# Optimization experiments

Hardware: AMD Instinct MI355X
Metric: run time of the kernel (lower is better)

The kernel has to match this reference:

```python
import jax, jax.numpy as jnp
import numpy as np

INPUT_DIM = 2048
N_EXPERTS = 64
K = 2


def setup_inputs() -> dict:
    key = jax.random.key(0)
    kx, kw, kb = jax.random.split(key, 3)
    x = jax.random.normal(kx, (4, 4096, INPUT_DIM), dtype=jnp.float32)
    # nn.Linear(input_dim, n_experts): weight [n_experts, input_dim], bias [n_experts]
    bound = 1.0 / np.sqrt(INPUT_DIM)
    W = jax.random.uniform(kw, (N_EXPERTS, INPUT_DIM), minval=-bound, maxval=bound, dtype=jnp.float32)
    b = jax.random.uniform(kb, (N_EXPERTS,), minval=-bound, maxval=bound, dtype=jnp.float32)
    return {"x": x, "W": W, "b": b}


def reference(x, W, b):
    # logits: [B, S, E]
    logits = jnp.einsum('bsd,ed->bse', x, W) + b
    topk_vals, topk_indices = jax.lax.top_k(logits, K)  # over last (expert) axis
    gate_probs = jax.nn.softmax(topk_vals, axis=-1)
    return gate_probs, topk_indices
```

## Files before the change

kernel.cpp:

```cpp
#include <hip/hip_runtime.h>
#include <math.h>
#include <stdint.h>

typedef _Float16 half8 __attribute__((ext_vector_type(8)));
typedef float floatx4 __attribute__((ext_vector_type(4)));

#define NTOK   16384
#define DIM    2048
#define NEXP   64
#define MB     32
#define NBLK   (NTOK / MB)
#define KC     64
#define NCHUNK (DIM / KC)
#define WSW_H8 16384
#define WSW_BYTES (2 * WSW_H8 * 16)

#define A_BYTES 8192
#define B_BYTES 16384
#define AOFF(b) ((b) * A_BYTES)
#define BOFF(b) (2 * A_BYTES + (b) * B_BYTES)
#define SMEM_BYTES (2 * A_BYTES + 2 * B_BYTES)

__global__ void wprep_kernel(const float* __restrict__ W, _Float16* __restrict__ wsw) {
    const int id   = blockIdx.x * blockDim.x + threadIdx.x;
    const int lane = id & 63;
    const int tg   = (id >> 6) & 3;
    const int sg   = id >> 8;
    const int e    = tg * 16 + (lane & 15);
    const int k    = sg * 32 + (lane >> 4) * 8;
    const float* src = W + (size_t)e * DIM + k;
    half8 h, l;
#pragma unroll
    for (int j = 0; j < 8; j++) {
        const float v  = src[j];
        const _Float16 hh = (_Float16)v;
        h[j] = hh;
        l[j] = (_Float16)((v - (float)hh) * 2048.0f);
    }
    const size_t slot = (size_t)(sg * 4 + tg) * 64 + lane;
    ((half8*)wsw)[slot]          = h;
    ((half8*)wsw)[WSW_H8 + slot] = l;
}

__device__ __forceinline__ void split_a(const float4& v0, const float4& v1,
                                        half8& hi, half8& lo) {
    const float av[8] = {v0.x, v0.y, v0.z, v0.w, v1.x, v1.y, v1.z, v1.w};
#pragma unroll
    for (int j = 0; j < 8; j++) {
        const _Float16 hh = (_Float16)av[j];
        hi[j] = hh;
        lo[j] = (_Float16)((av[j] - (float)hh) * 2048.0f);
    }
}

__device__ __forceinline__ void dma16(const void* g, const char* l) {
    __builtin_amdgcn_global_load_lds(
        (const __attribute__((address_space(1))) unsigned int*)(uintptr_t)g,
        (__attribute__((address_space(3))) unsigned int*)(uintptr_t)l,
        16, 0, 0);
}

template <bool USE_WS>
__global__ __launch_bounds__(256, 3)
void gating_lds_kernel(const float* __restrict__ x, const float* __restrict__ W,
                       const _Float16* __restrict__ wsw, const float* __restrict__ bias,
                       float* __restrict__ out)
{
    __shared__ char smem[SMEM_BYTES];

    const int tid  = threadIdx.x;
    const int lane = tid & 63;
    const int w    = tid >> 6;
    const int mt   = w & 1;
    const int nh   = w >> 1;
    const int col  = lane & 15;
    const int quad = lane >> 4;
    const int tok0 = blockIdx.x * MB;
    const int m    = mt * 16 + col;

    const float* gA[2];
    unsigned     lA[2];
#pragma unroll
    for (int i = 0; i < 2; i++) {
        const int a   = w * 2 + i;
        const int row = a * 4 + (lane >> 4);
        const int pz  = lane & 15;
        const int gp  = (pz & 8) | ((pz & 7) ^ (row & 7));
        gA[i] = x + (size_t)(tok0 + row) * DIM + gp * 4;
        lA[i] = (unsigned)(a * 1024);
    }
    const half8* gB[4];
    unsigned     lB[4];
    if constexpr (USE_WS) {
#pragma unroll
        for (int j = 0; j < 4; j++) {
            const int b = w * 4 + j;
            const int split = b >> 3, idx = b & 7;
            gB[j] = (const half8*)wsw + (size_t)split * WSW_H8 + idx * 64 + lane;
            lB[j] = (unsigned)(split * 8192 + idx * 1024);
        }
    }

    floatx4 accm[2] = {{0,0,0,0},{0,0,0,0}};
    floatx4 accl[2] = {{0,0,0,0},{0,0,0,0}};

#pragma unroll
    for (int i = 0; i < 2; i++) dma16(gA[i], smem + AOFF(0) + lA[i]);
    if constexpr (USE_WS) {
#pragma unroll
        for (int j = 0; j < 4; j++) dma16(gB[j], smem + BOFF(0) + lB[j]);
    }

#pragma unroll 2
    for (int c = 0; c < NCHUNK; ++c) {
        __syncthreads();
        if (c + 1 < NCHUNK) {
            const int nb = (c + 1) & 1;
#pragma unroll
            for (int i = 0; i < 2; i++)
                dma16(gA[i] + (size_t)(c + 1) * KC, smem + AOFF(nb) + lA[i]);
            if constexpr (USE_WS) {
#pragma unroll
                for (int j = 0; j < 4; j++)
                    dma16(gB[j] + (size_t)(c + 1) * 512, smem + BOFF(nb) + lB[j]);
            }
        }
        const char* Ab = smem + AOFF(c & 1);
        const char* Bb = smem + BOFF(c & 1);
#pragma unroll
        for (int s = 0; s < 2; s++) {
            const float4 v0 = *(const float4*)(Ab + m * 256 + (8 * s + ((2 * quad + 0) ^ (m & 7))) * 16);
            const float4 v1 = *(const float4*)(Ab + m * 256 + (8 * s + ((2 * quad + 1) ^ (m & 7))) * 16);
            half8 ah, alo;
            split_a(v0, v1, ah, alo);
#pragma unroll
            for (int t = 0; t < 2; t++) {
                const int tg = nh * 2 + t;
                half8 bh, bl;
                if constexpr (USE_WS) {
                    bh = *(const half8*)(Bb + (s * 4 + tg) * 1024 + lane * 16);
                    bl = *(const half8*)(Bb + 8192 + (s * 4 + tg) * 1024 + lane * 16);
                } else {
                    const float* wr = W + (size_t)(tg * 16 + col) * DIM + c * KC + s * 32 + quad * 8;
                    split_a(*(const float4*)wr, *(const float4*)(wr + 4), bh, bl);
                }
                accm[t] = __builtin_amdgcn_mfma_f32_16x16x32_f16(ah,  bh, accm[t], 0, 0, 0);
                accl[t] = __builtin_amdgcn_mfma_f32_16x16x32_f16(ah,  bl, accl[t], 0, 0, 0);
                accl[t] = __builtin_amdgcn_mfma_f32_16x16x32_f16(alo, bh, accl[t], 0, 0, 0);
            }
        }
    }

    __syncthreads();
    float* lg = (float*)smem;
    const float inv = 1.0f / 2048.0f;
#pragma unroll
    for (int t = 0; t < 2; t++) {
        const int tg = nh * 2 + t;
#pragma unroll
        for (int r = 0; r < 4; r++) {
            lg[(mt * 16 + quad * 4 + r) * 65 + tg * 16 + col] = accm[t][r] + accl[t][r] * inv;
        }
    }
    __syncthreads();

    if (tid < MB) {
        const int t = tid;
        float v0 = -INFINITY, v1 = -INFINITY;
        int   i0 = 0, i1 = 0;
        for (int e = 0; e < NEXP; e++) {
            const float v = lg[t * 65 + e] + bias[e];
            if (v > v0) { v1 = v0; i1 = i0; v0 = v; i0 = e; }
            else if (v > v1) { v1 = v; i1 = e; }
        }
        const float e1 = expf(v1 - v0);
        const float sden = 1.f + e1;
        const int   g  = tok0 + t;
        out[2 * g + 0] = 1.f / sden;
        out[2 * g + 1] = e1 / sden;
        out[2 * NTOK + 2 * g + 0] = (float)i0;
        out[2 * NTOK + 2 * g + 1] = (float)i1;
    }
}

extern "C" void kernel_launch(void* const* d_in, const int* in_sizes, int n_in,
                              void* d_out, int out_size, void* d_ws, size_t ws_size,
                              hipStream_t stream) {
    const float* x    = (const float*)d_in[0];
    const float* W    = (const float*)d_in[1];
    const float* bias = (const float*)d_in[2];
    float*       out  = (float*)d_out;
    _Float16*    wsw  = (_Float16*)d_ws;

    if (ws_size >= (size_t)WSW_BYTES) {
        hipLaunchKernelGGL(wprep_kernel, dim3(64), dim3(256), 0, stream, (const float*)d_in[1], wsw);
        hipLaunchKernelGGL((gating_lds_kernel<true>), dim3(NBLK), dim3(256), 0, stream,
                           x, W, wsw, bias, out);
    } else {
        hipLaunchKernelGGL((gating_lds_kernel<false>), dim3(NBLK), dim3(256), 0, stream,
                           x, W, wsw, bias, out);
    }
}
```

Measured before the change: 207.1 us.

## Split K across waves with register-held W fragments and LDS reduction

Each block now handles 16 tokens, and each of its four waves owns a quarter of the K dimension across all 64 experts, instead of splitting tokens and experts among waves. The pre-split W fragments are loaded straight into registers with a one-chunk prefetch rather than staged through LDS. Per-wave x tiles are double-buffered with DMA and synchronized only by explicit vmcnt waits, so there are no block barriers inside the loop. Partial logits are reduced through LDS before the top-2 step. The aim is to remove per-chunk __syncthreads and LDS traffic for W, at the cost of more registers, twice as many blocks, redundant W reads per block, and fragile hand-counted vmcnt values.

```diff
diff --git a/kernel.cpp b/kernel.cpp
--- a/kernel.cpp
+++ b/kernel.cpp
@@ -8,18 +8,15 @@
 #define NTOK   16384
 #define DIM    2048
 #define NEXP   64
-#define MB     32
-#define NBLK   (NTOK / MB)
-#define KC     64
-#define NCHUNK (DIM / KC)
+#define TPB    16
+#define NBLK   (NTOK / TPB)
+#define NCHW   8
 #define WSW_H8 16384
 #define WSW_BYTES (2 * WSW_H8 * 16)
 
-#define A_BYTES 8192
-#define B_BYTES 16384
-#define AOFF(b) ((b) * A_BYTES)
-#define BOFF(b) (2 * A_BYTES + (b) * B_BYTES)
-#define SMEM_BYTES (2 * A_BYTES + 2 * B_BYTES)
+#define ABUF_BYTES 32768
+#define RED_STRIDE 68
+#define RED_F      (4 * 16 * RED_STRIDE)
 
 __global__ void wprep_kernel(const float* __restrict__ W, _Float16* __restrict__ wsw) {
     const int id   = blockIdx.x * blockDim.x + threadIdx.x;
@@ -60,122 +57,137 @@
         16, 0, 0);
 }
 
+template <bool USE_WS> struct BFrag;
+template <> struct BFrag<true>  { half8  h[2][4]; half8 l[2][4]; };
+template <> struct BFrag<false> { float4 a[2][4][2]; };
+
+template <bool USE_WS>
+__device__ __forceinline__ void load_b(BFrag<USE_WS>& bf, const half8* wb,
+                                       const float* Wb, int cc) {
+    if constexpr (USE_WS) {
+#pragma unroll
+        for (int s = 0; s < 2; s++)
+#pragma unroll
+            for (int t = 0; t < 4; t++) {
+                const size_t o = (size_t)(cc * 8 + s * 4 + t) * 64;
+                bf.h[s][t] = wb[o];
+                bf.l[s][t] = wb[o + WSW_H8];
+            }
+    } else {
+#pragma unroll
+        for (int s = 0; s < 2; s++)
+#pragma unroll
+            for (int t = 0; t < 4; t++) {
+                const float* wr = Wb + (size_t)(t * 16) * DIM + cc * 64 + s * 32;
+                bf.a[s][t][0] = *(const float4*)wr;
+                bf.a[s][t][1] = *(const float4*)(wr + 4);
+            }
+    }
+}
+
 template <bool USE_WS>
 __global__ __launch_bounds__(256, 3)
-void gating_lds_kernel(const float* __restrict__ x, const float* __restrict__ W,
-                       const _Float16* __restrict__ wsw, const float* __restrict__ bias,
-                       float* __restrict__ out)
+void gating_kernel(const float* __restrict__ x, const float* __restrict__ W,
+                   const _Float16* __restrict__ wsw, const float* __restrict__ bias,
+                   float* __restrict__ out)
 {
-    __shared__ char smem[SMEM_BYTES];
+    __shared__ char  abuf[ABUF_BYTES];
+    __shared__ float red[RED_F];
 
     const int tid  = threadIdx.x;
     const int lane = tid & 63;
-    const int w    = tid >> 6;
-    const int mt   = w & 1;
-    const int nh   = w >> 1;
+    const int ks   = tid >> 6;
     const int col  = lane & 15;
     const int quad = lane >> 4;
-    const int tok0 = blockIdx.x * MB;
-    const int m    = mt * 16 + col;
-
-    const float* gA[2];
-    unsigned     lA[2];
-#pragma unroll
-    for (int i = 0; i < 2; i++) {
-        const int a   = w * 2 + i;
-        const int row = a * 4 + (lane >> 4);
-        const int pz  = lane & 15;
+    const int tok0 = blockIdx.x * TPB;
+
+    const float* gA[4];
+#pragma unroll
+    for (int i = 0; i < 4; i++) {
+        const int row = i * 4 + quad;
+        const int pz  = col;
         const int gp  = (pz & 8) | ((pz & 7) ^ (row & 7));
-        gA[i] = x + (size_t)(tok0 + row) * DIM + gp * 4;
-        lA[i] = (unsigned)(a * 1024);
-    }
-    const half8* gB[4];
-    unsigned     lB[4];
-    if constexpr (USE_WS) {
-#pragma unroll
-        for (int j = 0; j < 4; j++) {
-            const int b = w * 4 + j;
-            const int split = b >> 3, idx = b & 7;
-            gB[j] = (const half8*)wsw + (size_t)split * WSW_H8 + idx * 64 + lane;
-            lB[j] = (unsigned)(split * 8192 + idx * 1024);
-        }
-    }
-
-    floatx4 accm[2] = {{0,0,0,0},{0,0,0,0}};
-    floatx4 accl[2] = {{0,0,0,0},{0,0,0,0}};
-
-#pragma unroll
-    for (int i = 0; i < 2; i++) dma16(gA[i], smem + AOFF(0) + lA[i]);
-    if constexpr (USE_WS) {
-#pragma unroll
-        for (int j = 0; j < 4; j++) dma16(gB[j], smem + BOFF(0) + lB[j]);
-    }
-
-#pragma unroll 2
-    for (int c = 0; c < NCHUNK; ++c) {
-        __syncthreads();
-        if (c + 1 < NCHUNK) {
-            const int nb = (c + 1) & 1;
-#pragma unroll
-            for (int i = 0; i < 2; i++)
-                dma16(gA[i] + (size_t)(c + 1) * KC, smem + AOFF(nb) + lA[i]);
-            if constexpr (USE_WS) {
-#pragma unroll
-                for (int j = 0; j < 4; j++)
-                    dma16(gB[j] + (size_t)(c + 1) * 512, smem + BOFF(nb) + lB[j]);
-            }
-        }
-        const char* Ab = smem + AOFF(c & 1);
-        const char* Bb = smem + BOFF(c & 1);
+        gA[i] = x + (size_t)(tok0 + row) * DIM + ks * (NCHW * 64) + gp * 4;
+    }
+    char* const ab = abuf + ks * 8192;
+    const half8* wb = (const half8*)wsw + (size_t)ks * 4096 + lane;
+    const float* Wb = W + (size_t)col * DIM + ks * (NCHW * 64) + quad * 8;
+
+    floatx4 accm[4] = {{0,0,0,0},{0,0,0,0},{0,0,0,0},{0,0,0,0}};
+    floatx4 accl[4] = {{0,0,0,0},{0,0,0,0},{0,0,0,0},{0,0,0,0}};
+
+#pragma unroll
+    for (int i = 0; i < 4; i++) dma16(gA[i], ab + i * 1024);
+    asm volatile("" ::: "memory");
+    BFrag<USE_WS> bc;
+    load_b<USE_WS>(bc, wb, Wb, 0);
+#pragma unroll
+    for (int i = 0; i < 4; i++) dma16(gA[i] + 64, ab + 4096 + i * 1024);
+
+#pragma unroll
+    for (int cc = 0; cc < NCHW; ++cc) {
+        if (cc == NCHW - 1) asm volatile("s_waitcnt vmcnt(16)" ::: "memory");
+        else                asm volatile("s_waitcnt vmcnt(20)" ::: "memory");
+        const char* Ab = ab + (cc & 1) * 4096;
+        float4 v0[2], v1[2];
 #pragma unroll
         for (int s = 0; s < 2; s++) {
-            const float4 v0 = *(const float4*)(Ab + m * 256 + (8 * s + ((2 * quad + 0) ^ (m & 7))) * 16);
-            const float4 v1 = *(const float4*)(Ab + m * 256 + (8 * s + ((2 * quad + 1) ^ (m & 7))) * 16);
-            half8 ah, alo;
-            split_a(v0, v1, ah, alo);
-#pragma unroll
-            for (int t = 0; t < 2; t++) {
-                const int tg = nh * 2 + t;
+            v0[s] = *(const float4*)(Ab + col * 256 + (8 * s + ((2 * quad + 0) ^ (col & 7))) * 16);
+            v1[s] = *(const float4*)(Ab + col * 256 + (8 * s + ((2 * quad + 1) ^ (col & 7))) * 16);
+        }
+        asm volatile("s_waitcnt lgkmcnt(0)" ::: "memory");
+        BFrag<USE_WS> bn;
+        if (cc + 1 < NCHW) load_b<USE_WS>(bn, wb, Wb, cc + 1);
+        if (cc + 2 < NCHW) {
+#pragma unroll
+            for (int i = 0; i < 4; i++)
+                dma16(gA[i] + (size_t)(cc + 2) * 64, ab + (cc & 1) * 4096 + i * 1024);
+        }
+#pragma unroll
+        for (int s = 0; s < 2; s++) {
+            half8 ah, al;
+            split_a(v0[s], v1[s], ah, al);
+#pragma unroll
+            for (int t = 0; t < 4; t++) {
                 half8 bh, bl;
                 if constexpr (USE_WS) {
-                    bh = *(const half8*)(Bb + (s * 4 + tg) * 1024 + lane * 16);
-                    bl = *(const half8*)(Bb + 8192 + (s * 4 + tg) * 1024 + lane * 16);
+                    bh = bc.h[s][t];
+                    bl = bc.l[s][t];
                 } else {
-                    const float* wr = W + (size_t)(tg * 16 + col) * DIM + c * KC + s * 32 + quad * 8;
-                    split_a(*(const float4*)wr, *(const float4*)(wr + 4), bh, bl);
+                    split_a(bc.a[s][t][0], bc.a[s][t][1], bh, bl);
                 }
-                accm[t] = __builtin_amdgcn_mfma_f32_16x16x32_f16(ah,  bh, accm[t], 0, 0, 0);
-                accl[t] = __builtin_amdgcn_mfma_f32_16x16x32_f16(ah,  bl, accl[t], 0, 0, 0);
-                accl[t] = __builtin_amdgcn_mfma_f32_16x16x32_f16(alo, bh, accl[t], 0, 0, 0);
+                accm[t] = __builtin_amdgcn_mfma_f32_16x16x32_f16(ah, bh, accm[t], 0, 0, 0);
+                accl[t] = __builtin_amdgcn_mfma_f32_16x16x32_f16(ah, bl, accl[t], 0, 0, 0);
+                accl[t] = __builtin_amdgcn_mfma_f32_16x16x32_f16(al, bh, accl[t], 0, 0, 0);
             }
         }
-    }
-
+        if (cc + 1 < NCHW) bc = bn;
+    }
+
+    const float inv = 1.0f / 2048.0f;
+#pragma unroll
+    for (int t = 0; t < 4; t++)
+#pragma unroll
+        for (int r = 0; r < 4; r++)
+            red[(ks * 16 + quad * 4 + r) * RED_STRIDE + t * 16 + col] =
+                accm[t][r] + accl[t][r] * inv;
     __syncthreads();
-    float* lg = (float*)smem;
-    const float inv = 1.0f / 2048.0f;
-#pragma unroll
-    for (int t = 0; t < 2; t++) {
-        const int tg = nh * 2 + t;
-#pragma unroll
-        for (int r = 0; r < 4; r++) {
-            lg[(mt * 16 + quad * 4 + r) * 65 + tg * 16 + col] = accm[t][r] + accl[t][r] * inv;
-        }
-    }
-    __syncthreads();
-
-    if (tid < MB) {
-        const int t = tid;
+
+    if (tid < TPB) {
+        const int tk = tid;
         float v0 = -INFINITY, v1 = -INFINITY;
         int   i0 = 0, i1 = 0;
         for (int e = 0; e < NEXP; e++) {
-            const float v = lg[t * 65 + e] + bias[e];
-            if (v > v0) { v1 = v0; i1 = i0; v0 = v; i0 = e; }
+            const float v = red[(0 * 16 + tk) * RED_STRIDE + e]
+                          + red[(1 * 16 + tk) * RED_STRIDE + e]
+                          + red[(2 * 16 + tk) * RED_STRIDE + e]
+                          + red[(3 * 16 + tk) * RED_STRIDE + e] + bias[e];
+            if (v > v0)      { v1 = v0; i1 = i0; v0 = v; i0 = e; }
             else if (v > v1) { v1 = v; i1 = e; }
         }
         const float e1 = expf(v1 - v0);
         const float sden = 1.f + e1;
-        const int   g  = tok0 + t;
+        const int   g  = tok0 + tk;
         out[2 * g + 0] = 1.f / sden;
         out[2 * g + 1] = e1 / sden;
         out[2 * NTOK + 2 * g + 0] = (float)i0;
@@ -193,11 +205,11 @@
     _Float16*    wsw  = (_Float16*)d_ws;
 
     if (ws_size >= (size_t)WSW_BYTES) {
-        hipLaunchKernelGGL(wprep_kernel, dim3(64), dim3(256), 0, stream, (const float*)d_in[1], wsw);
-        hipLaunchKernelGGL((gating_lds_kernel<true>), dim3(NBLK), dim3(256), 0, stream,
+        hipLaunchKernelGGL(wprep_kernel, dim3(64), dim3(256), 0, stream, W, wsw);
+        hipLaunchKernelGGL((gating_kernel<true>), dim3(NBLK), dim3(256), 0, stream,
                            x, W, wsw, bias, out);
     } else {
-        hipLaunchKernelGGL((gating_lds_kernel<false>), dim3(NBLK), dim3(256), 0, stream,
+        hipLaunchKernelGGL((gating_kernel<false>), dim3(NBLK), dim3(256), 0, stream,
                            x, W, wsw, bias, out);
     }
 }
```

Measured after the change: 211.1 us. No clear change (+1.9%).

## Triple-buffer LDS chunks with prefetch distance two and vmcnt-based waits

Applied to the files above, without the earlier changes.

Expands the LDS staging from two to three buffers and issues DMA loads two chunks ahead. The full __syncthreads per chunk becomes a targeted s_waitcnt vmcnt plus s_barrier, so later loads stay in flight. The aim is to hide more global-memory latency when streaming x. In exchange, LDS use rises and launch bounds drop to two blocks per CU, which reduces occupancy.

```diff
diff --git a/kernel.cpp b/kernel.cpp
--- a/kernel.cpp
+++ b/kernel.cpp
@@ -18,8 +18,8 @@
 #define A_BYTES 8192
 #define B_BYTES 16384
 #define AOFF(b) ((b) * A_BYTES)
-#define BOFF(b) (2 * A_BYTES + (b) * B_BYTES)
-#define SMEM_BYTES (2 * A_BYTES + 2 * B_BYTES)
+#define BOFF(b) (3 * A_BYTES + (b) * B_BYTES)
+#define SMEM_BYTES (3 * A_BYTES + 3 * B_BYTES)
 
 __global__ void wprep_kernel(const float* __restrict__ W, _Float16* __restrict__ wsw) {
     const int id   = blockIdx.x * blockDim.x + threadIdx.x;
@@ -60,8 +60,13 @@
         16, 0, 0);
 }
 
+template <int N>
+__device__ __forceinline__ void wait_vm() {
+    asm volatile("s_waitcnt vmcnt(%0)" :: "n"(N) : "memory");
+}
+
 template <bool USE_WS>
-__global__ __launch_bounds__(256, 3)
+__global__ __launch_bounds__(256, 2)
 void gating_lds_kernel(const float* __restrict__ x, const float* __restrict__ W,
                        const _Float16* __restrict__ wsw, const float* __restrict__ bias,
                        float* __restrict__ out)
@@ -100,33 +105,43 @@
             lB[j] = (unsigned)(split * 8192 + idx * 1024);
         }
     }
+    constexpr int OPW = USE_WS ? 6 : 2;
 
     floatx4 accm[2] = {{0,0,0,0},{0,0,0,0}};
     floatx4 accl[2] = {{0,0,0,0},{0,0,0,0}};
 
 #pragma unroll
-    for (int i = 0; i < 2; i++) dma16(gA[i], smem + AOFF(0) + lA[i]);
-    if constexpr (USE_WS) {
-#pragma unroll
-        for (int j = 0; j < 4; j++) dma16(gB[j], smem + BOFF(0) + lB[j]);
-    }
-
-#pragma unroll 2
+    for (int c0 = 0; c0 < 2; c0++) {
+#pragma unroll
+        for (int i = 0; i < 2; i++)
+            dma16(gA[i] + (size_t)c0 * KC, smem + AOFF(c0) + lA[i]);
+        if constexpr (USE_WS) {
+#pragma unroll
+            for (int j = 0; j < 4; j++)
+                dma16(gB[j] + (size_t)c0 * 512, smem + BOFF(c0) + lB[j]);
+        }
+    }
+
+    int bi = 0, pi = 2;
     for (int c = 0; c < NCHUNK; ++c) {
-        __syncthreads();
-        if (c + 1 < NCHUNK) {
-            const int nb = (c + 1) & 1;
+        if (c < NCHUNK - 1) wait_vm<OPW>();
+        else                wait_vm<0>();
+        __builtin_amdgcn_s_barrier();
+        asm volatile("" ::: "memory");
+
+        if (c + 2 < NCHUNK) {
 #pragma unroll
             for (int i = 0; i < 2; i++)
-                dma16(gA[i] + (size_t)(c + 1) * KC, smem + AOFF(nb) + lA[i]);
+                dma16(gA[i] + (size_t)(c + 2) * KC, smem + AOFF(pi) + lA[i]);
             if constexpr (USE_WS) {
 #pragma unroll
                 for (int j = 0; j < 4; j++)
-                    dma16(gB[j] + (size_t)(c + 1) * 512, smem + BOFF(nb) + lB[j]);
+                    dma16(gB[j] + (size_t)(c + 2) * 512, smem + BOFF(pi) + lB[j]);
             }
         }
-        const char* Ab = smem + AOFF(c & 1);
-        const char* Bb = smem + BOFF(c & 1);
+
+        const char* Ab = smem + AOFF(bi);
+        const char* Bb = smem + BOFF(bi);
 #pragma unroll
         for (int s = 0; s < 2; s++) {
             const float4 v0 = *(const float4*)(Ab + m * 256 + (8 * s + ((2 * quad + 0) ^ (m & 7))) * 16);
@@ -149,6 +164,8 @@
                 accl[t] = __builtin_amdgcn_mfma_f32_16x16x32_f16(alo, bh, accl[t], 0, 0, 0);
             }
         }
+        bi = (bi == 2) ? 0 : bi + 1;
+        pi = (pi == 2) ? 0 : pi + 1;
     }
 
     __syncthreads();
@@ -193,7 +210,7 @@
     _Float16*    wsw  = (_Float16*)d_ws;
 
     if (ws_size >= (size_t)WSW_BYTES) {
-        hipLaunchKernelGGL(wprep_kernel, dim3(64), dim3(256), 0, stream, (const float*)d_in[1], wsw);
+        hipLaunchKernelGGL(wprep_kernel, dim3(64), dim3(256), 0, stream, W, wsw);
         hipLaunchKernelGGL((gating_lds_kernel<true>), dim3(NBLK), dim3(256), 0, stream,
                            x, W, wsw, bias, out);
     } else {
```

Result: no change. 208.6 us (+0.7%).
